# Kernel tuning notes

Hardware: AMD Instinct MI355X
Metric: run time of the kernel (lower is better)

The kernel has to match this reference:

```python
import jax, jax.numpy as jnp
import numpy as np

HEAD_COUNT = 6  # module scales by head_count**-0.5, not head_size
SCALE = HEAD_COUNT ** (-0.5)


def setup_inputs() -> dict:
    key = jax.random.key(0)
    kx, kq, kk, kv = jax.random.split(key, 4)
    B, T, C, H = 512, 128, 384, 64
    x = jax.random.normal(kx, (B, T, C), dtype=jnp.float32)
    init = (1.0 / np.sqrt(C)).astype(np.float32)
    Wq = jax.random.normal(kq, (C, H), dtype=jnp.float32) * init
    Wk = jax.random.normal(kk, (C, H), dtype=jnp.float32) * init
    Wv = jax.random.normal(kv, (C, H), dtype=jnp.float32) * init
    return {"x": x, "Wq": Wq, "Wk": Wk, "Wv": Wv}


def reference(x, Wq, Wk, Wv):
    # x: [B, T, C]; Wq/Wk/Wv: [C, H]
    q = jnp.einsum('btc,ch->bth', x, Wq)
    k = jnp.einsum('btc,ch->bth', x, Wk)
    v = jnp.einsum('btc,ch->bth', x, Wv)
    # scores: [B, T, T], scaled by head_count**-0.5 (faithful to source)
    scores = jnp.einsum('bth,bsh->bts', q, k) * SCALE
    T = x.shape[1]
    causal = jnp.tril(jnp.ones((T, T), dtype=bool))
    scores = jnp.where(causal, scores, -jnp.inf)
    weights = jax.nn.softmax(scores, axis=-1)
    # dropout omitted (eval mode / identity for reference baseline)
    return jnp.einsum('bts,bsh->bth', weights, v)
```

## Files before the change

### kernel.cpp

```cpp
#include <hip/hip_runtime.h>
#include <hip/hip_bf16.h>


#define B_ 512
#define T_ 128
#define C_ 384
#define H_ 64

typedef __bf16 bf16;
typedef __attribute__((ext_vector_type(8))) __bf16 bf16x8;
typedef __attribute__((ext_vector_type(4))) __bf16 bf16x4;
typedef __attribute__((ext_vector_type(4))) float f32x4;

#define GLOAD_LDS16(g, l)                                                     \
    __builtin_amdgcn_global_load_lds(                                         \
        (const __attribute__((address_space(1))) void*)(g),                   \
        (__attribute__((address_space(3))) void*)(l), 16, 0, 0)

__global__ void build_wt(const float* __restrict__ Wq, const float* __restrict__ Wk,
                         const float* __restrict__ Wv, bf16* __restrict__ Wt)
{
    int t = blockIdx.x * 256 + threadIdx.x;
    if (t >= 12 * 12 * 64) return;
    int lane = t & 63;
    int tn   = (t >> 6) % 12;
    int kc   = t / (12 * 64);
    int lm = lane & 15, quad = lane >> 4;
    int n = tn * 16 + lm;
    int j = n >> 6, h = n & 63;
    const float* Wp = (j == 0) ? Wq : (j == 1) ? Wk : Wv;
    int k0 = kc * 32 + quad * 8;
    bf16x8 v;
#pragma unroll
    for (int e = 0; e < 8; ++e) v[e] = (bf16)Wp[(k0 + e) * H_ + h];
    *(bf16x8*)&Wt[t * 8] = v;
}


__launch_bounds__(512, 4)
__global__ void head_fused(const float* __restrict__ x,
                           const bf16* __restrict__ Wt,
                           float* __restrict__ out)
{
    __shared__ __align__(16) bf16 lds[28672];
    bf16* Qs  = lds;
    bf16* Ks  = lds + 8192;
    bf16* Vts = lds + 16384;
    bf16* Ps  = lds;

    const int tid  = threadIdx.x;
    const int w    = tid >> 6;
    const int lane = tid & 63;
    const int lm   = lane & 15;
    const int quad = lane >> 4;
    const int mg   = w >> 2;
    const int ng   = w & 3;
    const int b    = blockIdx.x;

    const float* xb = x + (size_t)b * (T_ * C_);

    f32x4 acc[4][3];
#pragma unroll
    for (int mf = 0; mf < 4; ++mf)
#pragma unroll
        for (int nf = 0; nf < 3; ++nf) acc[mf][nf] = (f32x4){0.f, 0.f, 0.f, 0.f};

    const int r0 = tid >> 3, r1 = (tid + 512) >> 3;
    const float* gx0 = xb + (size_t)r0 * C_ + (((tid & 7) ^ (r0 & 7)) * 4);
    const float* gx1 = xb + (size_t)r1 * C_ + (((tid & 7) ^ (r1 & 7)) * 4);
    char* lx0 = (char*)lds + w * 1024;
    char* lx1 = (char*)lds + 8192 + w * 1024;
    const char* gwt = (const char*)Wt;
    char* lw0 = (char*)lds + 16384 + w * 1024;
    char* lw1 = (char*)lds + 16384 + 8192 + w * 1024;

    auto STAGE = [&](int kc) {
        int bo = (kc & 1) * 28672;
        GLOAD_LDS16(gx0 + kc * 32, lx0 + bo);
        GLOAD_LDS16(gx1 + kc * 32, lx1 + bo);
        GLOAD_LDS16(gwt + (size_t)kc * 12288 + tid * 16, lw0 + bo);
        if (w < 4)
            GLOAD_LDS16(gwt + (size_t)kc * 12288 + 8192 + tid * 16, lw1 + bo);
    };

    STAGE(0);
    asm volatile("s_waitcnt vmcnt(0)" ::: "memory");
    __builtin_amdgcn_s_barrier();

#pragma unroll
    for (int kc = 0; kc < 12; ++kc) {
        if (kc < 11) STAGE(kc + 1);

        const float* xc = (const float*)((const char*)lds + (kc & 1) * 28672);
        const bf16*  wc = (const bf16*)((const char*)lds + (kc & 1) * 28672 + 16384);

        bf16x8 afr[4];
#pragma unroll
        for (int mf = 0; mf < 4; ++mf) {
            int row = 64 * mg + 16 * mf + lm;
            int p0 = (2 * quad) ^ (row & 7);
            int p1 = (2 * quad + 1) ^ (row & 7);
            f32x4 va = *(const f32x4*)(xc + row * 32 + p0 * 4);
            f32x4 vb = *(const f32x4*)(xc + row * 32 + p1 * 4);
            afr[mf] = (bf16x8){(bf16)va[0], (bf16)va[1], (bf16)va[2], (bf16)va[3],
                               (bf16)vb[0], (bf16)vb[1], (bf16)vb[2], (bf16)vb[3]};
        }
#pragma unroll
        for (int nf = 0; nf < 3; ++nf) {
            bf16x8 bfr = *(const bf16x8*)(wc + (3 * ng + nf) * 512 + lane * 8);
#pragma unroll
            for (int mf = 0; mf < 4; ++mf)
                acc[mf][nf] =
                    __builtin_amdgcn_mfma_f32_16x16x32_bf16(afr[mf], bfr, acc[mf][nf], 0, 0, 0);
        }

        if (kc < 11) {
            asm volatile("s_waitcnt vmcnt(0)" ::: "memory");
            __builtin_amdgcn_s_barrier();
        }
    }
    __syncthreads();

#pragma unroll
    for (int mf = 0; mf < 4; ++mf) {
#pragma unroll
        for (int nf = 0; nf < 3; ++nf) {
            int tn = 3 * ng + nf;
            int gn = 16 * tn + lm;
            int j = gn >> 6, h = gn & 63;
            int m0 = 64 * mg + 16 * mf + quad * 4;
            if (j == 2) {
                bf16x4 v4 = {(bf16)acc[mf][nf][0], (bf16)acc[mf][nf][1],
                             (bf16)acc[mf][nf][2], (bf16)acc[mf][nf][3]};
                int pc = (m0 & 7) | ((((m0 >> 3) ^ (h & 15)) & 15) << 3);
                *(bf16x4*)&Vts[h * 128 + pc] = v4;
            } else {
                bf16* dst = (j == 0) ? Qs : Ks;
#pragma unroll
                for (int r = 0; r < 4; ++r) {
                    int m = m0 + r;
                    int pc = (h & 7) | ((((h >> 3) ^ (m & 7)) & 7) << 3);
                    dst[m * 64 + pc] = (bf16)acc[mf][nf][r];
                }
            }
        }
    }
    __syncthreads();

    const float SCALE = 0.40824829046386307f;
    const int tm = w;
    const int mrow = 16 * tm + lm;

    f32x4 sacc[8];
#pragma unroll
    for (int t = 0; t < 8; ++t) sacc[t] = (f32x4){0.f, 0.f, 0.f, 0.f};

    bf16x8 qa[2];
#pragma unroll
    for (int ks = 0; ks < 2; ++ks) {
        int phys = ((ks * 4 + quad) ^ (mrow & 7)) & 7;
        qa[ks] = *(const bf16x8*)&Qs[mrow * 64 + phys * 8];
    }
#pragma unroll
    for (int tn = 0; tn < 8; ++tn) {
        if (tn <= tm) {
            int nrow = 16 * tn + lm;
#pragma unroll
            for (int ks = 0; ks < 2; ++ks) {
                int phys = ((ks * 4 + quad) ^ (nrow & 7)) & 7;
                bf16x8 kb = *(const bf16x8*)&Ks[nrow * 64 + phys * 8];
                sacc[tn] =
                    __builtin_amdgcn_mfma_f32_16x16x32_bf16(qa[ks], kb, sacc[tn], 0, 0, 0);
            }
        }
    }

#pragma unroll
    for (int r = 0; r < 4; ++r) {
        int m = 16 * tm + quad * 4 + r;
        float mx = -1e30f;
#pragma unroll
        for (int tn = 0; tn < 8; ++tn) {
            if (tn <= tm) {
                int n = 16 * tn + lm;
                float v = (n <= m) ? sacc[tn][r] * SCALE : -1e30f;
                sacc[tn][r] = v;
                mx = fmaxf(mx, v);
            }
        }
#pragma unroll
        for (int off = 1; off < 16; off <<= 1) mx = fmaxf(mx, __shfl_xor(mx, off, 16));
        float sum = 0.f;
#pragma unroll
        for (int tn = 0; tn < 8; ++tn) {
            if (tn <= tm) {
                float e = __expf(sacc[tn][r] - mx);
                sacc[tn][r] = e;
                sum += e;
            }
        }
#pragma unroll
        for (int off = 1; off < 16; off <<= 1) sum += __shfl_xor(sum, off, 16);
        float inv = 1.f / sum;
#pragma unroll
        for (int tn = 0; tn < 8; ++tn) {
            if (tn <= tm) sacc[tn][r] *= inv;
        }
    }

    __syncthreads();

#pragma unroll
    for (int tn = 0; tn < 8; ++tn) {
        if (tn <= tm) {
            int n = 16 * tn + lm;
#pragma unroll
            for (int r = 0; r < 4; ++r) {
                int m = 16 * tm + quad * 4 + r;
                int pc = (n & 7) | ((((n >> 3) ^ (m & 15)) & 15) << 3);
                Ps[m * 128 + pc] = (bf16)sacc[tn][r];
            }
        }
    }
    if ((tm & 1) == 0) {
        int m = 16 * tm + lm;
        int c0 = 16 * (tm + 1) + quad * 4;
        int pc = (c0 & 7) | ((((c0 >> 3) ^ (m & 15)) & 15) << 3);
        *(bf16x4*)&Ps[m * 128 + pc] =
            (bf16x4){(bf16)0.f, (bf16)0.f, (bf16)0.f, (bf16)0.f};
    }

    f32x4 oacc[4];
#pragma unroll
    for (int t = 0; t < 4; ++t) oacc[t] = (f32x4){0.f, 0.f, 0.f, 0.f};

    const int nks = (tm + 2) >> 1;
    for (int ks = 0; ks < nks; ++ks) {
        int unit = ks * 4 + quad;
        int phys = (unit ^ (mrow & 15)) & 15;
        bf16x8 pa = *(const bf16x8*)&Ps[mrow * 128 + phys * 8];
#pragma unroll
        for (int th = 0; th < 4; ++th) {
            int hrow = 16 * th + lm;
            int ph2 = (unit ^ (hrow & 15)) & 15;
            bf16x8 vb = *(const bf16x8*)&Vts[hrow * 128 + ph2 * 8];
            oacc[th] =
                __builtin_amdgcn_mfma_f32_16x16x32_bf16(pa, vb, oacc[th], 0, 0, 0);
        }
    }

    float* ob = out + (size_t)b * (T_ * H_);
#pragma unroll
    for (int th = 0; th < 4; ++th) {
        int h = 16 * th + lm;
#pragma unroll
        for (int r = 0; r < 4; ++r) {
            int m = 16 * tm + quad * 4 + r;
            ob[m * 64 + h] = oacc[th][r];
        }
    }
}

extern "C" void kernel_launch(void* const* d_in, const int* in_sizes, int n_in,
                              void* d_out, int out_size, void* d_ws, size_t ws_size,
                              hipStream_t stream) {
    const float* x  = (const float*)d_in[0];
    const float* Wq = (const float*)d_in[1];
    const float* Wk = (const float*)d_in[2];
    const float* Wv = (const float*)d_in[3];
    float* o = (float*)d_out;
    bf16* Wt = (bf16*)d_ws;
    build_wt<<<dim3(36), dim3(256), 0, stream>>>(Wq, Wk, Wv, Wt);
    head_fused<<<dim3(B_), dim3(512), 0, stream>>>(x, Wt, o);
}
```

Before: 168.2 us.

## Split fused head kernel into QKV GEMM and attention kernels via workspace

The single fused kernel is split into two launches. The first computes the Q, K and V projections and writes the swizzled LDS image (48 KB per batch, bf16) to a global workspace. The second loads that image back into LDS and runs the causal attention. This separates the register-heavy GEMM phase from the attention phase, at the cost of an extra global round-trip of about 25 MB and one more launch. The fused kernel is kept as a fallback when the workspace is too small.

```diff
diff --git a/kernel.cpp b/kernel.cpp
--- a/kernel.cpp
+++ b/kernel.cpp
@@ -36,17 +36,15 @@
     *(bf16x8*)&Wt[t * 8] = v;
 }
 
-
 __launch_bounds__(512, 4)
-__global__ void head_fused(const float* __restrict__ x,
-                           const bf16* __restrict__ Wt,
-                           float* __restrict__ out)
+__global__ void qkv_gemm(const float* __restrict__ x,
+                         const bf16* __restrict__ Wt,
+                         bf16* __restrict__ qkv)
 {
     __shared__ __align__(16) bf16 lds[28672];
     bf16* Qs  = lds;
     bf16* Ks  = lds + 8192;
     bf16* Vts = lds + 16384;
-    bf16* Ps  = lds;
 
     const int tid  = threadIdx.x;
     const int w    = tid >> 6;
@@ -147,6 +145,263 @@
     }
     __syncthreads();
 
+    char* dst = (char*)qkv + (size_t)b * 49152;
+    const char* ldsb = (const char*)lds;
+#pragma unroll
+    for (int u = 0; u < 6; ++u) {
+        int off = (u * 512 + tid) * 16;
+        *(float4*)(dst + off) = *(const float4*)(ldsb + off);
+    }
+}
+
+__launch_bounds__(512, 4)
+__global__ void attn(const bf16* __restrict__ qkv, float* __restrict__ out)
+{
+    __shared__ __align__(16) bf16 lds[24576];
+    bf16* Qs  = lds;
+    bf16* Ks  = lds + 8192;
+    bf16* Vts = lds + 16384;
+    bf16* Ps  = lds;
+
+    const int tid  = threadIdx.x;
+    const int w    = tid >> 6;
+    const int lane = tid & 63;
+    const int lm   = lane & 15;
+    const int quad = lane >> 4;
+    const int b    = blockIdx.x;
+
+    const char* src = (const char*)qkv + (size_t)b * 49152;
+    char* ldsb = (char*)lds + w * 1024;
+#pragma unroll
+    for (int u = 0; u < 6; ++u)
+        GLOAD_LDS16(src + (u * 512 + tid) * 16, ldsb + u * 8192);
+    asm volatile("s_waitcnt vmcnt(0)" ::: "memory");
+    __syncthreads();
+
+    const float SCALE = 0.40824829046386307f;
+    const int tm = w;
+    const int mrow = 16 * tm + lm;
+
+    f32x4 sacc[8];
+#pragma unroll
+    for (int t = 0; t < 8; ++t) sacc[t] = (f32x4){0.f, 0.f, 0.f, 0.f};
+
+    bf16x8 qa[2];
+#pragma unroll
+    for (int ks = 0; ks < 2; ++ks) {
+        int phys = ((ks * 4 + quad) ^ (mrow & 7)) & 7;
+        qa[ks] = *(const bf16x8*)&Qs[mrow * 64 + phys * 8];
+    }
+#pragma unroll
+    for (int tn = 0; tn < 8; ++tn) {
+        if (tn <= tm) {
+            int nrow = 16 * tn + lm;
+#pragma unroll
+            for (int ks = 0; ks < 2; ++ks) {
+                int phys = ((ks * 4 + quad) ^ (nrow & 7)) & 7;
+                bf16x8 kb = *(const bf16x8*)&Ks[nrow * 64 + phys * 8];
+                sacc[tn] =
+                    __builtin_amdgcn_mfma_f32_16x16x32_bf16(qa[ks], kb, sacc[tn], 0, 0, 0);
+            }
+        }
+    }
+
+#pragma unroll
+    for (int r = 0; r < 4; ++r) {
+        int m = 16 * tm + quad * 4 + r;
+        float mx = -1e30f;
+#pragma unroll
+        for (int tn = 0; tn < 8; ++tn) {
+            if (tn <= tm) {
+                int n = 16 * tn + lm;
+                float v = (n <= m) ? sacc[tn][r] * SCALE : -1e30f;
+                sacc[tn][r] = v;
+                mx = fmaxf(mx, v);
+            }
+        }
+#pragma unroll
+        for (int off = 1; off < 16; off <<= 1) mx = fmaxf(mx, __shfl_xor(mx, off, 16));
+        float sum = 0.f;
+#pragma unroll
+        for (int tn = 0; tn < 8; ++tn) {
+            if (tn <= tm) {
+                float e = __expf(sacc[tn][r] - mx);
+                sacc[tn][r] = e;
+                sum += e;
+            }
+        }
+#pragma unroll
+        for (int off = 1; off < 16; off <<= 1) sum += __shfl_xor(sum, off, 16);
+        float inv = 1.f / sum;
+#pragma unroll
+        for (int tn = 0; tn < 8; ++tn) {
+            if (tn <= tm) sacc[tn][r] *= inv;
+        }
+    }
+
+    __syncthreads();
+
+#pragma unroll
+    for (int tn = 0; tn < 8; ++tn) {
+        if (tn <= tm) {
+            int n = 16 * tn + lm;
+#pragma unroll
+            for (int r = 0; r < 4; ++r) {
+                int m = 16 * tm + quad * 4 + r;
+                int pc = (n & 7) | ((((n >> 3) ^ (m & 15)) & 15) << 3);
+                Ps[m * 128 + pc] = (bf16)sacc[tn][r];
+            }
+        }
+    }
+    if ((tm & 1) == 0) {
+        int m = 16 * tm + lm;
+        int c0 = 16 * (tm + 1) + quad * 4;
+        int pc = (c0 & 7) | ((((c0 >> 3) ^ (m & 15)) & 15) << 3);
+        *(bf16x4*)&Ps[m * 128 + pc] =
+            (bf16x4){(bf16)0.f, (bf16)0.f, (bf16)0.f, (bf16)0.f};
+    }
+
+    f32x4 oacc[4];
+#pragma unroll
+    for (int t = 0; t < 4; ++t) oacc[t] = (f32x4){0.f, 0.f, 0.f, 0.f};
+
+    const int nks = (tm + 2) >> 1;
+    for (int ks = 0; ks < nks; ++ks) {
+        int unit = ks * 4 + quad;
+        int phys = (unit ^ (mrow & 15)) & 15;
+        bf16x8 pa = *(const bf16x8*)&Ps[mrow * 128 + phys * 8];
+#pragma unroll
+        for (int th = 0; th < 4; ++th) {
+            int hrow = 16 * th + lm;
+            int ph2 = (unit ^ (hrow & 15)) & 15;
+            bf16x8 vb = *(const bf16x8*)&Vts[hrow * 128 + ph2 * 8];
+            oacc[th] =
+                __builtin_amdgcn_mfma_f32_16x16x32_bf16(pa, vb, oacc[th], 0, 0, 0);
+        }
+    }
+
+    float* ob = out + (size_t)b * (T_ * H_);
+#pragma unroll
+    for (int th = 0; th < 4; ++th) {
+        int h = 16 * th + lm;
+#pragma unroll
+        for (int r = 0; r < 4; ++r) {
+            int m = 16 * tm + quad * 4 + r;
+            ob[m * 64 + h] = oacc[th][r];
+        }
+    }
+}
+
+__launch_bounds__(512, 4)
+__global__ void head_fused(const float* __restrict__ x,
+                           const bf16* __restrict__ Wt,
+                           float* __restrict__ out)
+{
+    __shared__ __align__(16) bf16 lds[28672];
+    bf16* Qs  = lds;
+    bf16* Ks  = lds + 8192;
+    bf16* Vts = lds + 16384;
+    bf16* Ps  = lds;
+
+    const int tid  = threadIdx.x;
+    const int w    = tid >> 6;
+    const int lane = tid & 63;
+    const int lm   = lane & 15;
+    const int quad = lane >> 4;
+    const int mg   = w >> 2;
+    const int ng   = w & 3;
+    const int b    = blockIdx.x;
+
+    const float* xb = x + (size_t)b * (T_ * C_);
+
+    f32x4 acc[4][3];
+#pragma unroll
+    for (int mf = 0; mf < 4; ++mf)
+#pragma unroll
+        for (int nf = 0; nf < 3; ++nf) acc[mf][nf] = (f32x4){0.f, 0.f, 0.f, 0.f};
+
+    const int r0 = tid >> 3, r1 = (tid + 512) >> 3;
+    const float* gx0 = xb + (size_t)r0 * C_ + (((tid & 7) ^ (r0 & 7)) * 4);
+    const float* gx1 = xb + (size_t)r1 * C_ + (((tid & 7) ^ (r1 & 7)) * 4);
+    char* lx0 = (char*)lds + w * 1024;
+    char* lx1 = (char*)lds + 8192 + w * 1024;
+    const char* gwt = (const char*)Wt;
+    char* lw0 = (char*)lds + 16384 + w * 1024;
+    char* lw1 = (char*)lds + 16384 + 8192 + w * 1024;
+
+    auto STAGE = [&](int kc) {
+        int bo = (kc & 1) * 28672;
+        GLOAD_LDS16(gx0 + kc * 32, lx0 + bo);
+        GLOAD_LDS16(gx1 + kc * 32, lx1 + bo);
+        GLOAD_LDS16(gwt + (size_t)kc * 12288 + tid * 16, lw0 + bo);
+        if (w < 4)
+            GLOAD_LDS16(gwt + (size_t)kc * 12288 + 8192 + tid * 16, lw1 + bo);
+    };
+
+    STAGE(0);
+    asm volatile("s_waitcnt vmcnt(0)" ::: "memory");
+    __builtin_amdgcn_s_barrier();
+
+#pragma unroll
+    for (int kc = 0; kc < 12; ++kc) {
+        if (kc < 11) STAGE(kc + 1);
+
+        const float* xc = (const float*)((const char*)lds + (kc & 1) * 28672);
+        const bf16*  wc = (const bf16*)((const char*)lds + (kc & 1) * 28672 + 16384);
+
+        bf16x8 afr[4];
+#pragma unroll
+        for (int mf = 0; mf < 4; ++mf) {
+            int row = 64 * mg + 16 * mf + lm;
+            int p0 = (2 * quad) ^ (row & 7);
+            int p1 = (2 * quad + 1) ^ (row & 7);
+            f32x4 va = *(const f32x4*)(xc + row * 32 + p0 * 4);
+            f32x4 vb = *(const f32x4*)(xc + row * 32 + p1 * 4);
+            afr[mf] = (bf16x8){(bf16)va[0], (bf16)va[1], (bf16)va[2], (bf16)va[3],
+                               (bf16)vb[0], (bf16)vb[1], (bf16)vb[2], (bf16)vb[3]};
+        }
+#pragma unroll
+        for (int nf = 0; nf < 3; ++nf) {
+            bf16x8 bfr = *(const bf16x8*)(wc + (3 * ng + nf) * 512 + lane * 8);
+#pragma unroll
+            for (int mf = 0; mf < 4; ++mf)
+                acc[mf][nf] =
+                    __builtin_amdgcn_mfma_f32_16x16x32_bf16(afr[mf], bfr, acc[mf][nf], 0, 0, 0);
+        }
+
+        if (kc < 11) {
+            asm volatile("s_waitcnt vmcnt(0)" ::: "memory");
+            __builtin_amdgcn_s_barrier();
+        }
+    }
+    __syncthreads();
+
+#pragma unroll
+    for (int mf = 0; mf < 4; ++mf) {
+#pragma unroll
+        for (int nf = 0; nf < 3; ++nf) {
+            int tn = 3 * ng + nf;
+            int gn = 16 * tn + lm;
+            int j = gn >> 6, h = gn & 63;
+            int m0 = 64 * mg + 16 * mf + quad * 4;
+            if (j == 2) {
+                bf16x4 v4 = {(bf16)acc[mf][nf][0], (bf16)acc[mf][nf][1],
+                             (bf16)acc[mf][nf][2], (bf16)acc[mf][nf][3]};
+                int pc = (m0 & 7) | ((((m0 >> 3) ^ (h & 15)) & 15) << 3);
+                *(bf16x4*)&Vts[h * 128 + pc] = v4;
+            } else {
+                bf16* dst = (j == 0) ? Qs : Ks;
+#pragma unroll
+                for (int r = 0; r < 4; ++r) {
+                    int m = m0 + r;
+                    int pc = (h & 7) | ((((h >> 3) ^ (m & 7)) & 7) << 3);
+                    dst[m * 64 + pc] = (bf16)acc[mf][nf][r];
+                }
+            }
+        }
+    }
+    __syncthreads();
+
     const float SCALE = 0.40824829046386307f;
     const int tm = w;
     const int mrow = 16 * tm + lm;
@@ -270,6 +525,15 @@
     const float* Wv = (const float*)d_in[3];
     float* o = (float*)d_out;
     bf16* Wt = (bf16*)d_ws;
+    const size_t WT_BYTES  = 147456;
+    const size_t QKV_BYTES = (size_t)B_ * 49152;
+
     build_wt<<<dim3(36), dim3(256), 0, stream>>>(Wq, Wk, Wv, Wt);
-    head_fused<<<dim3(B_), dim3(512), 0, stream>>>(x, Wt, o);
+    if (ws_size >= WT_BYTES + QKV_BYTES) {
+        bf16* qkv = (bf16*)((char*)d_ws + WT_BYTES);
+        qkv_gemm<<<dim3(B_), dim3(512), 0, stream>>>(x, Wt, qkv);
+        attn<<<dim3(B_), dim3(512), 0, stream>>>(qkv, o);
+    } else {
+        head_fused<<<dim3(B_), dim3(512), 0, stream>>>(x, Wt, o);
+    }
 }
```

Result: slower. 177.4 us (+5.5%).

## Process two batches per block to share weight tile loads

Applied to the files above, without the earlier changes.

Each workgroup now handles two batch elements, staging both x tiles and one shared weight tile per k-step. The two batches' MFMAs reuse the same B fragments, and attention runs sequentially per batch in separate LDS regions. This halves the grid and raises LDS use and register pressure (launch bounds lowered to 2), trading occupancy and parallelism for less weight traffic.

```diff
diff --git a/kernel.cpp b/kernel.cpp
--- a/kernel.cpp
+++ b/kernel.cpp
@@ -37,16 +37,12 @@
 }
 
 
-__launch_bounds__(512, 4)
+__launch_bounds__(512, 2)
 __global__ void head_fused(const float* __restrict__ x,
                            const bf16* __restrict__ Wt,
                            float* __restrict__ out)
 {
-    __shared__ __align__(16) bf16 lds[28672];
-    bf16* Qs  = lds;
-    bf16* Ks  = lds + 8192;
-    bf16* Vts = lds + 16384;
-    bf16* Ps  = lds;
+    __shared__ __align__(16) bf16 lds[49152];
 
     const int tid  = threadIdx.x;
     const int w    = tid >> 6;
@@ -55,32 +51,42 @@
     const int quad = lane >> 4;
     const int mg   = w >> 2;
     const int ng   = w & 3;
-    const int b    = blockIdx.x;
-
-    const float* xb = x + (size_t)b * (T_ * C_);
-
-    f32x4 acc[4][3];
-#pragma unroll
-    for (int mf = 0; mf < 4; ++mf)
-#pragma unroll
-        for (int nf = 0; nf < 3; ++nf) acc[mf][nf] = (f32x4){0.f, 0.f, 0.f, 0.f};
+    const int b0   = 2 * blockIdx.x;
+
+    const float* xb0 = x + (size_t)b0 * (T_ * C_);
+    const float* xb1 = xb0 + (T_ * C_);
+
+    f32x4 acc[2][4][3];
+#pragma unroll
+    for (int g = 0; g < 2; ++g)
+#pragma unroll
+        for (int mf = 0; mf < 4; ++mf)
+#pragma unroll
+            for (int nf = 0; nf < 3; ++nf) acc[g][mf][nf] = (f32x4){0.f, 0.f, 0.f, 0.f};
 
     const int r0 = tid >> 3, r1 = (tid + 512) >> 3;
-    const float* gx0 = xb + (size_t)r0 * C_ + (((tid & 7) ^ (r0 & 7)) * 4);
-    const float* gx1 = xb + (size_t)r1 * C_ + (((tid & 7) ^ (r1 & 7)) * 4);
-    char* lx0 = (char*)lds + w * 1024;
-    char* lx1 = (char*)lds + 8192 + w * 1024;
+    const int c0 = ((tid & 7) ^ (r0 & 7)) * 4, c1 = ((tid & 7) ^ (r1 & 7)) * 4;
+    const float* g0a = xb0 + (size_t)r0 * C_ + c0;
+    const float* g0b = xb0 + (size_t)r1 * C_ + c1;
+    const float* g1a = xb1 + (size_t)r0 * C_ + c0;
+    const float* g1b = xb1 + (size_t)r1 * C_ + c1;
+    char* l0a = (char*)lds + w * 1024;
+    char* l0b = (char*)lds + 8192 + w * 1024;
+    char* l1a = (char*)lds + 16384 + w * 1024;
+    char* l1b = (char*)lds + 24576 + w * 1024;
     const char* gwt = (const char*)Wt;
-    char* lw0 = (char*)lds + 16384 + w * 1024;
-    char* lw1 = (char*)lds + 16384 + 8192 + w * 1024;
+    char* lwa = (char*)lds + 32768 + w * 1024;
+    char* lwb = (char*)lds + 32768 + 8192 + w * 1024;
 
     auto STAGE = [&](int kc) {
-        int bo = (kc & 1) * 28672;
-        GLOAD_LDS16(gx0 + kc * 32, lx0 + bo);
-        GLOAD_LDS16(gx1 + kc * 32, lx1 + bo);
-        GLOAD_LDS16(gwt + (size_t)kc * 12288 + tid * 16, lw0 + bo);
+        int bo = (kc & 1) * 45056;
+        GLOAD_LDS16(g0a + kc * 32, l0a + bo);
+        GLOAD_LDS16(g0b + kc * 32, l0b + bo);
+        GLOAD_LDS16(g1a + kc * 32, l1a + bo);
+        GLOAD_LDS16(g1b + kc * 32, l1b + bo);
+        GLOAD_LDS16(gwt + (size_t)kc * 12288 + tid * 16, lwa + bo);
         if (w < 4)
-            GLOAD_LDS16(gwt + (size_t)kc * 12288 + 8192 + tid * 16, lw1 + bo);
+            GLOAD_LDS16(gwt + (size_t)kc * 12288 + 8192 + tid * 16, lwb + bo);
     };
 
     STAGE(0);
@@ -91,27 +97,40 @@
     for (int kc = 0; kc < 12; ++kc) {
         if (kc < 11) STAGE(kc + 1);
 
-        const float* xc = (const float*)((const char*)lds + (kc & 1) * 28672);
-        const bf16*  wc = (const bf16*)((const char*)lds + (kc & 1) * 28672 + 16384);
-
-        bf16x8 afr[4];
+        const char* bufc = (const char*)lds + (kc & 1) * 45056;
+        const float* xc0 = (const float*)bufc;
+        const float* xc1 = (const float*)(bufc + 16384);
+        const bf16*  wc  = (const bf16*)(bufc + 32768);
+
+        bf16x8 bfr[3];
+#pragma unroll
+        for (int nf = 0; nf < 3; ++nf)
+            bfr[nf] = *(const bf16x8*)(wc + (3 * ng + nf) * 512 + lane * 8);
+
+        bf16x8 afr0[4], afr1[4];
 #pragma unroll
         for (int mf = 0; mf < 4; ++mf) {
             int row = 64 * mg + 16 * mf + lm;
             int p0 = (2 * quad) ^ (row & 7);
             int p1 = (2 * quad + 1) ^ (row & 7);
-            f32x4 va = *(const f32x4*)(xc + row * 32 + p0 * 4);
-            f32x4 vb = *(const f32x4*)(xc + row * 32 + p1 * 4);
-            afr[mf] = (bf16x8){(bf16)va[0], (bf16)va[1], (bf16)va[2], (bf16)va[3],
-                               (bf16)vb[0], (bf16)vb[1], (bf16)vb[2], (bf16)vb[3]};
+            f32x4 va = *(const f32x4*)(xc0 + row * 32 + p0 * 4);
+            f32x4 vb = *(const f32x4*)(xc0 + row * 32 + p1 * 4);
+            afr0[mf] = (bf16x8){(bf16)va[0], (bf16)va[1], (bf16)va[2], (bf16)va[3],
+                                (bf16)vb[0], (bf16)vb[1], (bf16)vb[2], (bf16)vb[3]};
+            f32x4 vc = *(const f32x4*)(xc1 + row * 32 + p0 * 4);
+            f32x4 vd = *(const f32x4*)(xc1 + row * 32 + p1 * 4);
+            afr1[mf] = (bf16x8){(bf16)vc[0], (bf16)vc[1], (bf16)vc[2], (bf16)vc[3],
+                                (bf16)vd[0], (bf16)vd[1], (bf16)vd[2], (bf16)vd[3]};
         }
 #pragma unroll
         for (int nf = 0; nf < 3; ++nf) {
-            bf16x8 bfr = *(const bf16x8*)(wc + (3 * ng + nf) * 512 + lane * 8);
-#pragma unroll
-            for (int mf = 0; mf < 4; ++mf)
-                acc[mf][nf] =
-                    __builtin_amdgcn_mfma_f32_16x16x32_bf16(afr[mf], bfr, acc[mf][nf], 0, 0, 0);
+#pragma unroll
+            for (int mf = 0; mf < 4; ++mf) {
+                acc[0][mf][nf] = __builtin_amdgcn_mfma_f32_16x16x32_bf16(
+                    afr0[mf], bfr[nf], acc[0][mf][nf], 0, 0, 0);
+                acc[1][mf][nf] = __builtin_amdgcn_mfma_f32_16x16x32_bf16(
+                    afr1[mf], bfr[nf], acc[1][mf][nf], 0, 0, 0);
+            }
         }
 
         if (kc < 11) {
@@ -122,25 +141,32 @@
     __syncthreads();
 
 #pragma unroll
-    for (int mf = 0; mf < 4; ++mf) {
-#pragma unroll
-        for (int nf = 0; nf < 3; ++nf) {
-            int tn = 3 * ng + nf;
-            int gn = 16 * tn + lm;
-            int j = gn >> 6, h = gn & 63;
-            int m0 = 64 * mg + 16 * mf + quad * 4;
-            if (j == 2) {
-                bf16x4 v4 = {(bf16)acc[mf][nf][0], (bf16)acc[mf][nf][1],
-                             (bf16)acc[mf][nf][2], (bf16)acc[mf][nf][3]};
-                int pc = (m0 & 7) | ((((m0 >> 3) ^ (h & 15)) & 15) << 3);
-                *(bf16x4*)&Vts[h * 128 + pc] = v4;
-            } else {
-                bf16* dst = (j == 0) ? Qs : Ks;
-#pragma unroll
-                for (int r = 0; r < 4; ++r) {
-                    int m = m0 + r;
-                    int pc = (h & 7) | ((((h >> 3) ^ (m & 7)) & 7) << 3);
-                    dst[m * 64 + pc] = (bf16)acc[mf][nf][r];
+    for (int g = 0; g < 2; ++g) {
+        bf16* img = lds + g * 24576;
+        bf16* Qs  = img;
+        bf16* Ks  = img + 8192;
+        bf16* Vts = img + 16384;
+#pragma unroll
+        for (int mf = 0; mf < 4; ++mf) {
+#pragma unroll
+            for (int nf = 0; nf < 3; ++nf) {
+                int tn = 3 * ng + nf;
+                int gn = 16 * tn + lm;
+                int j = gn >> 6, h = gn & 63;
+                int m0 = 64 * mg + 16 * mf + quad * 4;
+                if (j == 2) {
+                    bf16x4 v4 = {(bf16)acc[g][mf][nf][0], (bf16)acc[g][mf][nf][1],
+                                 (bf16)acc[g][mf][nf][2], (bf16)acc[g][mf][nf][3]};
+                    int pc = (m0 & 7) | ((((m0 >> 3) ^ (h & 15)) & 15) << 3);
+                    *(bf16x4*)&Vts[h * 128 + pc] = v4;
+                } else {
+                    bf16* dst = (j == 0) ? Qs : Ks;
+#pragma unroll
+                    for (int r = 0; r < 4; ++r) {
+                        int m = m0 + r;
+                        int pc = (h & 7) | ((((h >> 3) ^ (m & 7)) & 7) << 3);
+                        dst[m * 64 + pc] = (bf16)acc[g][mf][nf][r];
+                    }
                 }
             }
         }
@@ -151,112 +177,121 @@
     const int tm = w;
     const int mrow = 16 * tm + lm;
 
-    f32x4 sacc[8];
-#pragma unroll
-    for (int t = 0; t < 8; ++t) sacc[t] = (f32x4){0.f, 0.f, 0.f, 0.f};
-
-    bf16x8 qa[2];
-#pragma unroll
-    for (int ks = 0; ks < 2; ++ks) {
-        int phys = ((ks * 4 + quad) ^ (mrow & 7)) & 7;
-        qa[ks] = *(const bf16x8*)&Qs[mrow * 64 + phys * 8];
-    }
-#pragma unroll
-    for (int tn = 0; tn < 8; ++tn) {
-        if (tn <= tm) {
-            int nrow = 16 * tn + lm;
-#pragma unroll
-            for (int ks = 0; ks < 2; ++ks) {
-                int phys = ((ks * 4 + quad) ^ (nrow & 7)) & 7;
-                bf16x8 kb = *(const bf16x8*)&Ks[nrow * 64 + phys * 8];
-                sacc[tn] =
-                    __builtin_amdgcn_mfma_f32_16x16x32_bf16(qa[ks], kb, sacc[tn], 0, 0, 0);
-            }
-        }
-    }
-
-#pragma unroll
-    for (int r = 0; r < 4; ++r) {
-        int m = 16 * tm + quad * 4 + r;
-        float mx = -1e30f;
+#pragma unroll
+    for (int g = 0; g < 2; ++g) {
+        bf16* img = lds + g * 24576;
+        bf16* Qs  = img;
+        bf16* Ks  = img + 8192;
+        bf16* Vts = img + 16384;
+        bf16* Ps  = img;
+
+        f32x4 sacc[8];
+#pragma unroll
+        for (int t = 0; t < 8; ++t) sacc[t] = (f32x4){0.f, 0.f, 0.f, 0.f};
+
+        bf16x8 qa[2];
+#pragma unroll
+        for (int ks = 0; ks < 2; ++ks) {
+            int phys = ((ks * 4 + quad) ^ (mrow & 7)) & 7;
+            qa[ks] = *(const bf16x8*)&Qs[mrow * 64 + phys * 8];
+        }
+#pragma unroll
+        for (int tn = 0; tn < 8; ++tn) {
+            if (tn <= tm) {
+                int nrow = 16 * tn + lm;
+#pragma unroll
+                for (int ks = 0; ks < 2; ++ks) {
+                    int phys = ((ks * 4 + quad) ^ (nrow & 7)) & 7;
+                    bf16x8 kb = *(const bf16x8*)&Ks[nrow * 64 + phys * 8];
+                    sacc[tn] =
+                        __builtin_amdgcn_mfma_f32_16x16x32_bf16(qa[ks], kb, sacc[tn], 0, 0, 0);
+                }
+            }
+        }
+
+#pragma unroll
+        for (int r = 0; r < 4; ++r) {
+            int m = 16 * tm + quad * 4 + r;
+            float mx = -1e30f;
+#pragma unroll
+            for (int tn = 0; tn < 8; ++tn) {
+                if (tn <= tm) {
+                    int n = 16 * tn + lm;
+                    float v = (n <= m) ? sacc[tn][r] * SCALE : -1e30f;
+                    sacc[tn][r] = v;
+                    mx = fmaxf(mx, v);
+                }
+            }
+#pragma unroll
+            for (int off = 1; off < 16; off <<= 1) mx = fmaxf(mx, __shfl_xor(mx, off, 16));
+            float sum = 0.f;
+#pragma unroll
+            for (int tn = 0; tn < 8; ++tn) {
+                if (tn <= tm) {
+                    float e = __expf(sacc[tn][r] - mx);
+                    sacc[tn][r] = e;
+                    sum += e;
+                }
+            }
+#pragma unroll
+            for (int off = 1; off < 16; off <<= 1) sum += __shfl_xor(sum, off, 16);
+            float inv = 1.f / sum;
+#pragma unroll
+            for (int tn = 0; tn < 8; ++tn) {
+                if (tn <= tm) sacc[tn][r] *= inv;
+            }
+        }
+
+        __syncthreads();
+
 #pragma unroll
         for (int tn = 0; tn < 8; ++tn) {
             if (tn <= tm) {
                 int n = 16 * tn + lm;
-                float v = (n <= m) ? sacc[tn][r] * SCALE : -1e30f;
-                sacc[tn][r] = v;
-                mx = fmaxf(mx, v);
-            }
-        }
-#pragma unroll
-        for (int off = 1; off < 16; off <<= 1) mx = fmaxf(mx, __shfl_xor(mx, off, 16));
-        float sum = 0.f;
-#pragma unroll
-        for (int tn = 0; tn < 8; ++tn) {
-            if (tn <= tm) {
-                float e = __expf(sacc[tn][r] - mx);
-                sacc[tn][r] = e;
-                sum += e;
-            }
-        }
-#pragma unroll
-        for (int off = 1; off < 16; off <<= 1) sum += __shfl_xor(sum, off, 16);
-        float inv = 1.f / sum;
-#pragma unroll
-        for (int tn = 0; tn < 8; ++tn) {
-            if (tn <= tm) sacc[tn][r] *= inv;
-        }
-    }
-
-    __syncthreads();
-
-#pragma unroll
-    for (int tn = 0; tn < 8; ++tn) {
-        if (tn <= tm) {
-            int n = 16 * tn + lm;
+#pragma unroll
+                for (int r = 0; r < 4; ++r) {
+                    int m = 16 * tm + quad * 4 + r;
+                    int pc = (n & 7) | ((((n >> 3) ^ (m & 15)) & 15) << 3);
+                    Ps[m * 128 + pc] = (bf16)sacc[tn][r];
+                }
+            }
+        }
+        if ((tm & 1) == 0) {
+            int m = 16 * tm + lm;
+            int cc = 16 * (tm + 1) + quad * 4;
+            int pc = (cc & 7) | ((((cc >> 3) ^ (m & 15)) & 15) << 3);
+            *(bf16x4*)&Ps[m * 128 + pc] =
+                (bf16x4){(bf16)0.f, (bf16)0.f, (bf16)0.f, (bf16)0.f};
+        }
+
+        f32x4 oacc[4];
+#pragma unroll
+        for (int t = 0; t < 4; ++t) oacc[t] = (f32x4){0.f, 0.f, 0.f, 0.f};
+
+        const int nks = (tm + 2) >> 1;
+        for (int ks = 0; ks < nks; ++ks) {
+            int unit = ks * 4 + quad;
+            int phys = (unit ^ (mrow & 15)) & 15;
+            bf16x8 pa = *(const bf16x8*)&Ps[mrow * 128 + phys * 8];
+#pragma unroll
+            for (int th = 0; th < 4; ++th) {
+                int hrow = 16 * th + lm;
+                int ph2 = (unit ^ (hrow & 15)) & 15;
+                bf16x8 vb = *(const bf16x8*)&Vts[hrow * 128 + ph2 * 8];
+                oacc[th] =
+                    __builtin_amdgcn_mfma_f32_16x16x32_bf16(pa, vb, oacc[th], 0, 0, 0);
+            }
+        }
+
+        float* ob = out + (size_t)(b0 + g) * (T_ * H_);
+#pragma unroll
+        for (int th = 0; th < 4; ++th) {
+            int h = 16 * th + lm;
 #pragma unroll
             for (int r = 0; r < 4; ++r) {
                 int m = 16 * tm + quad * 4 + r;
-                int pc = (n & 7) | ((((n >> 3) ^ (m & 15)) & 15) << 3);
-                Ps[m * 128 + pc] = (bf16)sacc[tn][r];
-            }
-        }
-    }
-    if ((tm & 1) == 0) {
-        int m = 16 * tm + lm;
-        int c0 = 16 * (tm + 1) + quad * 4;
-        int pc = (c0 & 7) | ((((c0 >> 3) ^ (m & 15)) & 15) << 3);
-        *(bf16x4*)&Ps[m * 128 + pc] =
-            (bf16x4){(bf16)0.f, (bf16)0.f, (bf16)0.f, (bf16)0.f};
-    }
-
-    f32x4 oacc[4];
-#pragma unroll
-    for (int t = 0; t < 4; ++t) oacc[t] = (f32x4){0.f, 0.f, 0.f, 0.f};
-
-    const int nks = (tm + 2) >> 1;
-    for (int ks = 0; ks < nks; ++ks) {
-        int unit = ks * 4 + quad;
-        int phys = (unit ^ (mrow & 15)) & 15;
-        bf16x8 pa = *(const bf16x8*)&Ps[mrow * 128 + phys * 8];
-#pragma unroll
-        for (int th = 0; th < 4; ++th) {
-            int hrow = 16 * th + lm;
-            int ph2 = (unit ^ (hrow & 15)) & 15;
-            bf16x8 vb = *(const bf16x8*)&Vts[hrow * 128 + ph2 * 8];
-            oacc[th] =
-                __builtin_amdgcn_mfma_f32_16x16x32_bf16(pa, vb, oacc[th], 0, 0, 0);
-        }
-    }
-
-    float* ob = out + (size_t)b * (T_ * H_);
-#pragma unroll
-    for (int th = 0; th < 4; ++th) {
-        int h = 16 * th + lm;
-#pragma unroll
-        for (int r = 0; r < 4; ++r) {
-            int m = 16 * tm + quad * 4 + r;
-            ob[m * 64 + h] = oacc[th][r];
+                ob[m * 64 + h] = oacc[th][r];
+            }
         }
     }
 }
@@ -271,5 +306,5 @@
     float* o = (float*)d_out;
     bf16* Wt = (bf16*)d_ws;
     build_wt<<<dim3(36), dim3(256), 0, stream>>>(Wq, Wk, Wv, Wt);
-    head_fused<<<dim3(B_), dim3(512), 0, stream>>>(x, Wt, o);
+    head_fused<<<dim3(B_ / 2), dim3(512), 0, stream>>>(x, Wt, o);
 }
```

Result: slower. 173.2 us (+3.0%).
